# Kernel optimization log

Hardware: AMD Instinct MI355X
Metric: run time of the kernel (lower is better)

## Reference

```python
import jax, jax.numpy as jnp
import numpy as np

B, N, FIN, FOUT, K = 8, 1024, 32, 4, 2
FREQS = [2.0, 3.0, 4.0, 5.0]  # q_idx = 1/FREQS[idx]


def setup_inputs() -> dict:
    key = jax.random.key(0)
    k1, k2, k3, k4, k5 = jax.random.split(key, 5)
    X_real = jax.random.normal(k1, (B, N, FIN), jnp.float32)
    X_imag = jax.random.normal(k2, (B, N, FIN), jnp.float32)
    adj = jax.random.uniform(k3, (B, N, N), jnp.float32)  # weighted directed adjacency
    stdv = 1.0 / np.sqrt(FIN)
    weight = jax.random.uniform(k4, (FOUT, K + 1, FIN), jnp.float32, -stdv, stdv)
    bias = jax.random.uniform(k5, (FOUT,), jnp.float32, -stdv, stdv)
    return {"X_real": X_real, "X_imag": X_imag, "adj": adj, "weight": weight, "bias": bias}


def _mag_laplacian(adj, q):
    """Normalized magnetic Laplacian, real/imag parts. adj: [B,N,N]."""
    adj_t = jnp.swapaxes(adj, -1, -2)
    As = 0.5 * (adj + adj_t)                    # symmetrized adjacency
    D = As.sum(-1)                              # degrees [B,N]
    dinv = jnp.where(D > 0, 1.0 / jnp.sqrt(jnp.where(D > 0, D, 1.0)), 0.0)
    theta = (2.0 * np.pi * q) * (adj - adj_t)   # phase matrix
    S = dinv[:, :, None] * As * dinv[:, None, :]  # D^-1/2 As D^-1/2
    I = jnp.eye(N, dtype=adj.dtype)
    L_real = I - S * jnp.cos(theta)
    L_imag = -S * jnp.sin(theta)
    return L_real, L_imag


def _cmatvec(Lr, Li, zr, zi):
    """Complex batched matmul (Lr+iLi) @ (zr+izi); L:[B,N,N], z:[B,N,F]."""
    return Lr @ zr - Li @ zi, Li @ zr + Lr @ zi


def reference(X_real, X_imag, adj, weight, bias):
    outs_r, outs_i = [], []
    for idx in range(FOUT):  # small fixed loop over output channels / frequencies
        q = 1.0 / FREQS[idx]
        Lr, Li = _mag_laplacian(adj, q)
        # Chebyshev polynomials applied directly to the signal:
        # T0 = I -> z0 = X ; T1 = I - L -> z1 = X - L X ; T_k = 2 L T_{k-1} + T_{k-2}
        z = [(X_real, X_imag)]
        hr, hi = _cmatvec(Lr, Li, X_real, X_imag)
        z.append((X_real - hr, X_imag - hi))
        for i in range(2, K + 1):
            mr, mi = _cmatvec(Lr, Li, z[i - 1][0], z[i - 1][1])
            z.append((2.0 * mr + z[i - 2][0], 2.0 * mi + z[i - 2][1]))
        Zr = jnp.stack([t[0] for t in z], 0)  # [K+1, B, N, FIN]
        Zi = jnp.stack([t[1] for t in z], 0)
        or_ = jnp.einsum('kbnf,kf->bn', Zr, weight[idx]) + bias[idx]
        oi_ = jnp.einsum('kbnf,kf->bn', Zi, weight[idx])
        outs_r.append(or_)
        outs_i.append(oi_)
    return jnp.stack(outs_r, -1), jnp.stack(outs_i, -1)  # each [B, N, FOUT]
```

## Files before the change

### kernel.cpp

```cpp
#include <hip/hip_runtime.h>
#include <cstddef>

#define NB 8
#define NN 1024
#define NF 32
#define NIDX 4
#define JC 4
#define JCH 256
#define NJT 4
#define TIB 32

#define OFF_ROW   0u
#define OFF_COLP  8192u
#define OFF_DINV  532480u
#define OFF_P     540672u
#define OFF_R     606208u
#define OFF_WT    671744u
#define OFF_WP    737280u

#if __has_builtin(__builtin_amdgcn_sinf)
#define FSIN(x) __builtin_amdgcn_sinf(x)
#define FCOS(x) __builtin_amdgcn_cosf(x)
#else
#define FSIN(x) __sinf((x) * 6.283185307179586f)
#define FCOS(x) __cosf((x) * 6.283185307179586f)
#endif

__global__ __launch_bounds__(512) void k_sums(const float* __restrict__ adj,
                                              float* __restrict__ rowsum,
                                              float* __restrict__ colpart) {
  int b = blockIdx.x, strip = blockIdx.y;
  int t = threadIdx.x, lane = t & 63, w = t >> 6;
  float colreg[16];
  #pragma unroll
  for (int i = 0; i < 16; ++i) colreg[i] = 0.f;
  int r0 = strip*16 + w*2;
  #pragma unroll
  for (int rr = 0; rr < 2; ++rr) {
    const float4* row4 = reinterpret_cast<const float4*>(adj + ((size_t)b*NN + r0 + rr)*NN);
    float rs = 0.f;
    #pragma unroll
    for (int cq = 0; cq < 4; ++cq) {
      float4 v = row4[cq*64 + lane];
      colreg[cq*4+0] += v.x; colreg[cq*4+1] += v.y;
      colreg[cq*4+2] += v.z; colreg[cq*4+3] += v.w;
      rs += (v.x + v.y) + (v.z + v.w);
    }
    #pragma unroll
    for (int o = 32; o > 0; o >>= 1) rs += __shfl_xor(rs, o);
    if (lane == 0) rowsum[b*NN + r0 + rr] = rs;
  }
  __shared__ float cacc[8][NN];
  #pragma unroll
  for (int cq = 0; cq < 4; ++cq)
    #pragma unroll
    for (int x = 0; x < 4; ++x) cacc[w][cq*256 + lane*4 + x] = colreg[cq*4+x];
  __syncthreads();
  for (int c = t; c < NN; c += 512) {
    float s = 0.f;
    #pragma unroll
    for (int ww = 0; ww < 8; ++ww) s += cacc[ww][c];
    colpart[(size_t)strip*(NB*NN) + b*NN + c] = s;
  }
}

__global__ __launch_bounds__(256) void k_prep(const float* __restrict__ Xr, const float* __restrict__ Xi,
                       const float* __restrict__ weight,
                       const float* __restrict__ rowsum, const float* __restrict__ colpart,
                       const float* __restrict__ bias,
                       float* __restrict__ dinv,
                       float* __restrict__ pvec, float* __restrict__ rvec,
                       float* __restrict__ out) {
  __shared__ float wsm[NIDX*3*NF];
  int t = threadIdx.x;
  for (int e = t; e < NIDX*3*NF; e += 256) wsm[e] = weight[e];
  __syncthreads();
  int gid = blockIdx.x*256 + t;
  float cs = 0.f;
  for (int k = 0; k < 64; ++k) cs += colpart[(size_t)k*(NB*NN) + gid];
  float D = 0.5f*(rowsum[gid] + cs);
  float di = (D > 0.f) ? (1.0f / sqrtf(D)) : 0.f;
  dinv[gid] = di;
  const float* xr = Xr + (size_t)gid*NF;
  const float* xi = Xi + (size_t)gid*NF;
  float acc[NIDX][3][2];
  #pragma unroll
  for (int x = 0; x < NIDX; ++x)
    #pragma unroll
    for (int v = 0; v < 3; ++v) { acc[x][v][0] = 0.f; acc[x][v][1] = 0.f; }
  for (int f = 0; f < NF; ++f) {
    float xrf = xr[f], xif = xi[f];
    #pragma unroll
    for (int x = 0; x < NIDX; ++x) {
      float w0 = wsm[x*96 + f], w1 = wsm[x*96 + 32 + f], w2 = wsm[x*96 + 64 + f];
      float av = w0 + w2, bv = w1 + 2.f*w2, cv = -2.f*w2;
      acc[x][0][0] += av*xrf; acc[x][0][1] += av*xif;
      acc[x][1][0] += bv*xrf; acc[x][1][1] += bv*xif;
      acc[x][2][0] += cv*xrf; acc[x][2][1] += cv*xif;
    }
  }
  #pragma unroll
  for (int x = 0; x < NIDX; ++x) {
    size_t o = (size_t)gid*8 + x*2;
    pvec[o] = acc[x][1][0];      pvec[o+1] = acc[x][1][1];
    rvec[o] = di*acc[x][2][0];   rvec[o+1] = di*acc[x][2][1];
    out[gid*4 + x]         = acc[x][0][0] + bias[x];
    out[32768 + gid*4 + x] = acc[x][0][1];
  }
}

__global__ void k_mid(const float* __restrict__ dinv, const float* __restrict__ pvec,
                      const float* __restrict__ wpart, float* __restrict__ wtot) {
  int o = blockIdx.x*256 + threadIdx.x;
  float v = pvec[o];
  #pragma unroll
  for (int c = 0; c < JC; ++c) v += wpart[(size_t)c*65536 + o];
  wtot[o] = v * dinv[o >> 3];
}

template<int MODE>
__global__ __launch_bounds__(256, 4) void k_pass(const float* __restrict__ adj,
                                                 const float* __restrict__ dinv,
                                                 const float* __restrict__ vin,
                                                 float* __restrict__ outp) {
  __shared__ float red[4][8*72];
  int b = blockIdx.x, i0 = blockIdx.y*TIB, zc = blockIdx.z;
  int t = threadIdx.x, lane = t & 63, w = t >> 6;
  int wu = __builtin_amdgcn_readfirstlane(w);
  int ibase = i0 + wu*8;
  float accr[8][NIDX], acci[8][NIDX];
  #pragma unroll
  for (int s = 0; s < 8; ++s)
    #pragma unroll
    for (int x = 0; x < NIDX; ++x) { accr[s][x] = 0.f; acci[s][x] = 0.f; }

  for (int jt = 0; jt < NJT; ++jt) {
    int j0 = zc*JCH + jt*64;
    int jg = j0 + lane;
    const float4* acp = reinterpret_cast<const float4*>(adj + ((size_t)b*NN + jg)*NN + ibase);
    float4 ac0 = acp[0], ac1 = acp[1];
    const float4* vp = reinterpret_cast<const float4*>(vin + ((size_t)b*NN + jg)*8);
    float4 v0 = vp[0], v1 = vp[1];
    float vr[NIDX] = {v0.x, v0.z, v1.x, v1.z};
    float vi[NIDX] = {v0.y, v0.w, v1.y, v1.w};
    float acv[8] = {ac0.x, ac0.y, ac0.z, ac0.w, ac1.x, ac1.y, ac1.z, ac1.w};
    const float* arb = adj + ((size_t)b*NN + ibase)*NN + j0 + lane;
    #pragma unroll
    for (int s = 0; s < 8; ++s) {
      float ar = arb[(size_t)s*NN];
      float ac = acv[s];
      float dd = ar - ac, sm = ar + ac;
      float s4 = FSIN(0.25f*dd), c4 = FCOS(0.25f*dd);
      float s3 = FSIN((1.f/3.f)*dd), c3 = FCOS((1.f/3.f)*dd);
      float s5 = FSIN(0.2f*dd), c5 = FCOS(0.2f*dd);
      float c2 = 1.f - 2.f*s4*s4, s2 = 2.f*s4*c4;
      float csv[NIDX] = {c2, c3, c4, c5};
      float snv[NIDX] = {s2, s3, s4, s5};
      #pragma unroll
      for (int x = 0; x < NIDX; ++x) {
        float A = sm*csv[x], B = sm*snv[x];
        accr[s][x] += A*vr[x] - B*vi[x];
        acci[s][x] += A*vi[x] + B*vr[x];
      }
    }
  }

  bool b1 = (lane & 1), b2 = (lane & 2), b4 = (lane & 4);
  #pragma unroll
  for (int s = 0; s < 8; ++s) {
    float v0 = accr[s][0], v1 = acci[s][0], v2 = accr[s][1], v3 = acci[s][1];
    float v4 = accr[s][2], v5 = acci[s][2], v6 = accr[s][3], v7 = acci[s][3];
    float k0 = b1 ? v1 : v0, s0 = b1 ? v0 : v1;
    float k1 = b1 ? v3 : v2, s1 = b1 ? v2 : v3;
    float k2 = b1 ? v5 : v4, s2 = b1 ? v4 : v5;
    float k3 = b1 ? v7 : v6, s3 = b1 ? v6 : v7;
    v0 = k0 + __shfl_xor(s0, 1);
    v1 = k1 + __shfl_xor(s1, 1);
    v2 = k2 + __shfl_xor(s2, 1);
    v3 = k3 + __shfl_xor(s3, 1);
    k0 = b2 ? v1 : v0; s0 = b2 ? v0 : v1;
    k1 = b2 ? v3 : v2; s1 = b2 ? v2 : v3;
    v0 = k0 + __shfl_xor(s0, 2);
    v1 = k1 + __shfl_xor(s1, 2);
    k0 = b4 ? v1 : v0; s0 = b4 ? v0 : v1;
    v0 = k0 + __shfl_xor(s0, 4);
    red[w][s*72 + (lane & 7)*9 + (lane >> 3)] = v0;
  }
  __syncthreads();
  {
    int row = lane >> 3, slot = lane & 7;
    float sum = 0.f;
    #pragma unroll
    for (int g = 0; g < 8; ++g) sum += red[w][row*72 + slot*9 + g];
    int gi = b*NN + ibase + row;
    float val = sum * 0.5f * dinv[gi];
    if constexpr (MODE == 0) outp[(size_t)zc*65536 + (size_t)gi*8 + slot] = val;
    else atomicAdd(&outp[(slot & 1)*32768 + gi*4 + (slot >> 1)], val);
  }
}

extern "C" void kernel_launch(void* const* d_in, const int* in_sizes, int n_in,
                              void* d_out, int out_size, void* d_ws, size_t ws_size,
                              hipStream_t stream) {
  (void)in_sizes; (void)n_in; (void)out_size; (void)ws_size;
  const float* Xr     = (const float*)d_in[0];
  const float* Xi     = (const float*)d_in[1];
  const float* adj    = (const float*)d_in[2];
  const float* weight = (const float*)d_in[3];
  const float* bias   = (const float*)d_in[4];
  float* ws = (float*)d_ws;
  float* rowsum  = ws + OFF_ROW;
  float* colpart = ws + OFF_COLP;
  float* dinv    = ws + OFF_DINV;
  float* pvec    = ws + OFF_P;
  float* rvec    = ws + OFF_R;
  float* wtot    = ws + OFF_WT;
  float* wpart   = ws + OFF_WP;
  float* out = (float*)d_out;

  k_sums<<<dim3(NB, 64), 512, 0, stream>>>(adj, rowsum, colpart);
  k_prep<<<dim3(NB*NN/256), 256, 0, stream>>>(Xr, Xi, weight, rowsum, colpart, bias,
                                              dinv, pvec, rvec, out);
  k_pass<0><<<dim3(NB, NN/TIB, JC), 256, 0, stream>>>(adj, dinv, rvec, wpart);
  k_mid<<<dim3(256), 256, 0, stream>>>(dinv, pvec, wpart, wtot);
  k_pass<1><<<dim3(NB, NN/TIB, JC), 256, 0, stream>>>(adj, dinv, wtot, out);
}
```

Measured before the change: 54.94 us.

## Precompute symmetric sum/difference of adjacency as packed fp16 for both passes

A new pack kernel reads adjacency tiles and their transposes through shared memory, and writes a packed half2 (adj+adjT, adj-adjT) matrix. In the same pass it produces the degree partial sums, replacing the old row/column sum kernel. Both Chebyshev passes then read one 4-byte word per element with coalesced loads instead of two floats, one of them a strided transposed access. In exchange it adds an extra write and read of a 32 MB intermediate and loses precision by storing the phase difference and weight sum in fp16.

```diff
diff --git a/kernel.cpp b/kernel.cpp
--- a/kernel.cpp
+++ b/kernel.cpp
@@ -1,22 +1,22 @@
 #include <hip/hip_runtime.h>
+#include <hip/hip_fp16.h>
 #include <cstddef>
 
 #define NB 8
 #define NN 1024
 #define NF 32
 #define NIDX 4
+#define NTILE 16
+#define NPAIR 136
 #define JC 4
-#define JCH 256
-#define NJT 4
-#define TIB 32
-
-#define OFF_ROW   0u
-#define OFF_COLP  8192u
-#define OFF_DINV  532480u
-#define OFF_P     540672u
-#define OFF_R     606208u
-#define OFF_WT    671744u
-#define OFF_WP    737280u
+
+#define OFF_D     0u
+#define OFF_DINV  131072u
+#define OFF_SMDD  139264u
+#define OFF_P     8527872u
+#define OFF_R     8593408u
+#define OFF_WT    8658944u
+#define OFF_WP    8724480u
 
 #if __has_builtin(__builtin_amdgcn_sinf)
 #define FSIN(x) __builtin_amdgcn_sinf(x)
@@ -26,48 +26,98 @@
 #define FCOS(x) __cosf((x) * 6.283185307179586f)
 #endif
 
-__global__ __launch_bounds__(512) void k_sums(const float* __restrict__ adj,
-                                              float* __restrict__ rowsum,
-                                              float* __restrict__ colpart) {
-  int b = blockIdx.x, strip = blockIdx.y;
+#define TRIG6(dd, csv, snv)                                          \
+  float s4 = FSIN(0.25f*(dd)), c4w = FCOS(0.25f*(dd));               \
+  float s3 = FSIN((1.f/3.f)*(dd)), c3 = FCOS((1.f/3.f)*(dd));        \
+  float s5 = FSIN(0.2f*(dd)), c5 = FCOS(0.2f*(dd));                  \
+  float c2 = 1.f - 2.f*s4*s4, s2 = 2.f*s4*c4w;                       \
+  csv[0]=c2; csv[1]=c3; csv[2]=c4w; csv[3]=c5;                       \
+  snv[0]=s2; snv[1]=s3; snv[2]=s4; snv[3]=s5;
+
+#define TREDUCE(accr, acci, red, w, lane, b1, b2, b4)                \
+  _Pragma("unroll")                                                  \
+  for (int s = 0; s < 8; ++s) {                                      \
+    float v0 = accr[s][0], v1 = acci[s][0], v2 = accr[s][1], v3 = acci[s][1]; \
+    float v4 = accr[s][2], v5 = acci[s][2], v6 = accr[s][3], v7 = acci[s][3]; \
+    float k0 = b1 ? v1 : v0, s0 = b1 ? v0 : v1;                      \
+    float k1 = b1 ? v3 : v2, s1 = b1 ? v2 : v3;                      \
+    float k2 = b1 ? v5 : v4, s2_ = b1 ? v4 : v5;                     \
+    float k3 = b1 ? v7 : v6, s3_ = b1 ? v6 : v7;                     \
+    v0 = k0 + __shfl_xor(s0, 1);                                     \
+    v1 = k1 + __shfl_xor(s1, 1);                                     \
+    v2 = k2 + __shfl_xor(s2_, 1);                                    \
+    v3 = k3 + __shfl_xor(s3_, 1);                                    \
+    k0 = b2 ? v1 : v0; s0 = b2 ? v0 : v1;                            \
+    k1 = b2 ? v3 : v2; s1 = b2 ? v2 : v3;                            \
+    v0 = k0 + __shfl_xor(s0, 2);                                     \
+    v1 = k1 + __shfl_xor(s1, 2);                                     \
+    k0 = b4 ? v1 : v0; s0 = b4 ? v0 : v1;                            \
+    v0 = k0 + __shfl_xor(s0, 4);                                     \
+    red[w][s*72 + (lane & 7)*9 + (lane >> 3)] = v0;                  \
+  }
+
+__global__ __launch_bounds__(256, 4) void k_pack(const float* __restrict__ adj,
+                                                 unsigned* __restrict__ smdd,
+                                                 float* __restrict__ Dpart) {
+  __shared__ float As[64*65];
+  __shared__ float Bs[64*65];
+  int b = blockIdx.x;
+  int pid = blockIdx.y;
+  int ti = 0, rem = pid;
+  while (rem >= NTILE - ti) { rem -= NTILE - ti; ++ti; }
+  int tj = ti + rem;
+  bool diag = (ti == tj);
   int t = threadIdx.x, lane = t & 63, w = t >> 6;
-  float colreg[16];
-  #pragma unroll
-  for (int i = 0; i < 16; ++i) colreg[i] = 0.f;
-  int r0 = strip*16 + w*2;
-  #pragma unroll
-  for (int rr = 0; rr < 2; ++rr) {
-    const float4* row4 = reinterpret_cast<const float4*>(adj + ((size_t)b*NN + r0 + rr)*NN);
-    float rs = 0.f;
-    #pragma unroll
-    for (int cq = 0; cq < 4; ++cq) {
-      float4 v = row4[cq*64 + lane];
-      colreg[cq*4+0] += v.x; colreg[cq*4+1] += v.y;
-      colreg[cq*4+2] += v.z; colreg[cq*4+3] += v.w;
-      rs += (v.x + v.y) + (v.z + v.w);
-    }
-    #pragma unroll
-    for (int o = 32; o > 0; o >>= 1) rs += __shfl_xor(rs, o);
-    if (lane == 0) rowsum[b*NN + r0 + rr] = rs;
-  }
-  __shared__ float cacc[8][NN];
-  #pragma unroll
-  for (int cq = 0; cq < 4; ++cq)
-    #pragma unroll
-    for (int x = 0; x < 4; ++x) cacc[w][cq*256 + lane*4 + x] = colreg[cq*4+x];
+
+  #pragma unroll
+  for (int m = 0; m < 4; ++m) {
+    int e4 = t + 256*m;
+    int row = e4 >> 4, c4 = (e4 & 15) << 2;
+    float4 va = *reinterpret_cast<const float4*>(adj + ((size_t)b*NN + ti*64 + row)*NN + tj*64 + c4);
+    float* da = &As[row*65 + c4];
+    da[0] = va.x; da[1] = va.y; da[2] = va.z; da[3] = va.w;
+    if (!diag) {
+      float4 vb = *reinterpret_cast<const float4*>(adj + ((size_t)b*NN + tj*64 + row)*NN + ti*64 + c4);
+      float* db = &Bs[row*65 + c4];
+      db[0] = vb.x; db[1] = vb.y; db[2] = vb.z; db[3] = vb.w;
+    }
+  }
   __syncthreads();
-  for (int c = t; c < NN; c += 512) {
-    float s = 0.f;
-    #pragma unroll
-    for (int ww = 0; ww < 8; ++ww) s += cacc[ww][c];
-    colpart[(size_t)strip*(NB*NN) + b*NN + c] = s;
+
+  const float* Bp = diag ? As : Bs;
+  #pragma unroll
+  for (int m = 0; m < 16; ++m) {
+    int r = w + 4*m, c = lane;
+    float a  = As[r*65 + c];
+    float bt = Bp[c*65 + r];
+    float sm = a + bt, dd = a - bt;
+    __half2 h = __floats2half2_rn(sm, dd);
+    smdd[((size_t)b*NN + ti*64 + r)*NN + tj*64 + c] = *reinterpret_cast<unsigned*>(&h);
+    float rp = sm;
+    #pragma unroll
+    for (int o = 32; o > 0; o >>= 1) rp += __shfl_xor(rp, o);
+    if (lane == 0) Dpart[(size_t)tj*(NB*NN) + b*NN + ti*64 + r] = 0.5f*rp;
+  }
+  if (!diag) {
+    #pragma unroll
+    for (int m = 0; m < 16; ++m) {
+      int r = w + 4*m, c = lane;
+      float a  = Bs[r*65 + c];
+      float bt = As[c*65 + r];
+      float sm = a + bt, dd = a - bt;
+      __half2 h = __floats2half2_rn(sm, dd);
+      smdd[((size_t)b*NN + tj*64 + r)*NN + ti*64 + c] = *reinterpret_cast<unsigned*>(&h);
+      float rp = sm;
+      #pragma unroll
+      for (int o = 32; o > 0; o >>= 1) rp += __shfl_xor(rp, o);
+      if (lane == 0) Dpart[(size_t)ti*(NB*NN) + b*NN + tj*64 + r] = 0.5f*rp;
+    }
   }
 }
 
 __global__ __launch_bounds__(256) void k_prep(const float* __restrict__ Xr, const float* __restrict__ Xi,
                        const float* __restrict__ weight,
-                       const float* __restrict__ rowsum, const float* __restrict__ colpart,
-                       const float* __restrict__ bias,
+                       const float* __restrict__ Dpart, const float* __restrict__ bias,
                        float* __restrict__ dinv,
                        float* __restrict__ pvec, float* __restrict__ rvec,
                        float* __restrict__ out) {
@@ -76,9 +126,9 @@
   for (int e = t; e < NIDX*3*NF; e += 256) wsm[e] = weight[e];
   __syncthreads();
   int gid = blockIdx.x*256 + t;
-  float cs = 0.f;
-  for (int k = 0; k < 64; ++k) cs += colpart[(size_t)k*(NB*NN) + gid];
-  float D = 0.5f*(rowsum[gid] + cs);
+  float D = 0.f;
+  #pragma unroll
+  for (int k = 0; k < NTILE; ++k) D += Dpart[(size_t)k*(NB*NN) + gid];
   float di = (D > 0.f) ? (1.0f / sqrtf(D)) : 0.f;
   dinv[gid] = di;
   const float* xr = Xr + (size_t)gid*NF;
@@ -119,12 +169,12 @@
 }
 
 template<int MODE>
-__global__ __launch_bounds__(256, 4) void k_pass(const float* __restrict__ adj,
+__global__ __launch_bounds__(256, 4) void k_pass(const unsigned* __restrict__ smdd,
                                                  const float* __restrict__ dinv,
                                                  const float* __restrict__ vin,
                                                  float* __restrict__ outp) {
   __shared__ float red[4][8*72];
-  int b = blockIdx.x, i0 = blockIdx.y*TIB, zc = blockIdx.z;
+  int b = blockIdx.x, i0 = blockIdx.y*32, zc = blockIdx.z;
   int t = threadIdx.x, lane = t & 63, w = t >> 6;
   int wu = __builtin_amdgcn_readfirstlane(w);
   int ibase = i0 + wu*8;
@@ -134,28 +184,20 @@
     #pragma unroll
     for (int x = 0; x < NIDX; ++x) { accr[s][x] = 0.f; acci[s][x] = 0.f; }
 
-  for (int jt = 0; jt < NJT; ++jt) {
-    int j0 = zc*JCH + jt*64;
-    int jg = j0 + lane;
-    const float4* acp = reinterpret_cast<const float4*>(adj + ((size_t)b*NN + jg)*NN + ibase);
-    float4 ac0 = acp[0], ac1 = acp[1];
+  for (int jt = 0; jt < (NN/JC)/64; ++jt) {
+    int jg = zc*(NN/JC) + jt*64 + lane;
     const float4* vp = reinterpret_cast<const float4*>(vin + ((size_t)b*NN + jg)*8);
-    float4 v0 = vp[0], v1 = vp[1];
-    float vr[NIDX] = {v0.x, v0.z, v1.x, v1.z};
-    float vi[NIDX] = {v0.y, v0.w, v1.y, v1.w};
-    float acv[8] = {ac0.x, ac0.y, ac0.z, ac0.w, ac1.x, ac1.y, ac1.z, ac1.w};
-    const float* arb = adj + ((size_t)b*NN + ibase)*NN + j0 + lane;
+    float4 va = vp[0], vb = vp[1];
+    float vr[NIDX] = {va.x, va.z, vb.x, vb.z};
+    float vi[NIDX] = {va.y, va.w, vb.y, vb.w};
+    const unsigned* sp = smdd + ((size_t)b*NN + ibase)*NN + jg;
     #pragma unroll
     for (int s = 0; s < 8; ++s) {
-      float ar = arb[(size_t)s*NN];
-      float ac = acv[s];
-      float dd = ar - ac, sm = ar + ac;
-      float s4 = FSIN(0.25f*dd), c4 = FCOS(0.25f*dd);
-      float s3 = FSIN((1.f/3.f)*dd), c3 = FCOS((1.f/3.f)*dd);
-      float s5 = FSIN(0.2f*dd), c5 = FCOS(0.2f*dd);
-      float c2 = 1.f - 2.f*s4*s4, s2 = 2.f*s4*c4;
-      float csv[NIDX] = {c2, c3, c4, c5};
-      float snv[NIDX] = {s2, s3, s4, s5};
+      unsigned wrd = sp[(size_t)s*NN];
+      __half2 h = *reinterpret_cast<__half2*>(&wrd);
+      float sm = __low2float(h), dd = __high2float(h);
+      float csv[NIDX], snv[NIDX];
+      TRIG6(dd, csv, snv)
       #pragma unroll
       for (int x = 0; x < NIDX; ++x) {
         float A = sm*csv[x], B = sm*snv[x];
@@ -166,26 +208,7 @@
   }
 
   bool b1 = (lane & 1), b2 = (lane & 2), b4 = (lane & 4);
-  #pragma unroll
-  for (int s = 0; s < 8; ++s) {
-    float v0 = accr[s][0], v1 = acci[s][0], v2 = accr[s][1], v3 = acci[s][1];
-    float v4 = accr[s][2], v5 = acci[s][2], v6 = accr[s][3], v7 = acci[s][3];
-    float k0 = b1 ? v1 : v0, s0 = b1 ? v0 : v1;
-    float k1 = b1 ? v3 : v2, s1 = b1 ? v2 : v3;
-    float k2 = b1 ? v5 : v4, s2 = b1 ? v4 : v5;
-    float k3 = b1 ? v7 : v6, s3 = b1 ? v6 : v7;
-    v0 = k0 + __shfl_xor(s0, 1);
-    v1 = k1 + __shfl_xor(s1, 1);
-    v2 = k2 + __shfl_xor(s2, 1);
-    v3 = k3 + __shfl_xor(s3, 1);
-    k0 = b2 ? v1 : v0; s0 = b2 ? v0 : v1;
-    k1 = b2 ? v3 : v2; s1 = b2 ? v2 : v3;
-    v0 = k0 + __shfl_xor(s0, 2);
-    v1 = k1 + __shfl_xor(s1, 2);
-    k0 = b4 ? v1 : v0; s0 = b4 ? v0 : v1;
-    v0 = k0 + __shfl_xor(s0, 4);
-    red[w][s*72 + (lane & 7)*9 + (lane >> 3)] = v0;
-  }
+  TREDUCE(accr, acci, red, w, lane, b1, b2, b4)
   __syncthreads();
   {
     int row = lane >> 3, slot = lane & 7;
@@ -209,19 +232,19 @@
   const float* weight = (const float*)d_in[3];
   const float* bias   = (const float*)d_in[4];
   float* ws = (float*)d_ws;
-  float* rowsum  = ws + OFF_ROW;
-  float* colpart = ws + OFF_COLP;
+  float* Dpart   = ws + OFF_D;
   float* dinv    = ws + OFF_DINV;
+  unsigned* smdd = (unsigned*)(ws + OFF_SMDD);
   float* pvec    = ws + OFF_P;
   float* rvec    = ws + OFF_R;
   float* wtot    = ws + OFF_WT;
   float* wpart   = ws + OFF_WP;
   float* out = (float*)d_out;
 
-  k_sums<<<dim3(NB, 64), 512, 0, stream>>>(adj, rowsum, colpart);
-  k_prep<<<dim3(NB*NN/256), 256, 0, stream>>>(Xr, Xi, weight, rowsum, colpart, bias,
+  k_pack<<<dim3(NB, NPAIR), 256, 0, stream>>>(adj, smdd, Dpart);
+  k_prep<<<dim3(NB*NN/256), 256, 0, stream>>>(Xr, Xi, weight, Dpart, bias,
                                               dinv, pvec, rvec, out);
-  k_pass<0><<<dim3(NB, NN/TIB, JC), 256, 0, stream>>>(adj, dinv, rvec, wpart);
+  k_pass<0><<<dim3(NB, NN/32, JC), 256, 0, stream>>>(smdd, dinv, rvec, wpart);
   k_mid<<<dim3(256), 256, 0, stream>>>(dinv, pvec, wpart, wtot);
-  k_pass<1><<<dim3(NB, NN/TIB, JC), 256, 0, stream>>>(adj, dinv, wtot, out);
-}
+  k_pass<1><<<dim3(NB, NN/32, JC), 256, 0, stream>>>(smdd, dinv, wtot, out);
+}
```

Result: slower. 66.45 us (+21.0%).
